# Optimization experiments

Hardware: AMD Instinct MI355X
Metric: run time of the kernel (lower is better)

The kernel has to match this reference:

```python
import jax, jax.numpy as jnp
import numpy as np

H = 256      # hidden_dim
MEL = 80     # num_mel
R = 5        # reduction_factor
BS = 128
T_ENC = 512
T_DEC = 1000


def _gru_step(x, h, wih, whh, bih, bhh):
    # PyTorch GRU cell: gates order (r, z, n)
    gi = x @ wih.T + bih            # [bs, 3H]
    gh = h @ whh.T + bhh
    ir, iz, inn = jnp.split(gi, 3, axis=-1)
    hr, hz, hn = jnp.split(gh, 3, axis=-1)
    r = jax.nn.sigmoid(ir + hr)
    z = jax.nn.sigmoid(iz + hz)
    n = jnp.tanh(inn + r * hn)
    return (1.0 - z) * n + z * h


def setup_inputs() -> dict:
    key = jax.random.key(0)
    ks = iter(jax.random.split(key, 40))
    s = 0.05
    def w(shape):
        return jax.random.normal(next(ks), shape, dtype=jnp.float32) * s
    inp = {
        "enc_vec": jax.random.normal(next(ks), (BS, T_ENC, H), dtype=jnp.float32),
        "decoder_input": jax.random.normal(next(ks), (BS, T_DEC, MEL), dtype=jnp.float32),
        # Pre_net
        "pre_w1": w((H, MEL)), "pre_b1": jnp.zeros((H,), jnp.float32),
        "pre_w2": w((H // 2, H)), "pre_b2": jnp.zeros((H // 2,), jnp.float32),
        # Bahdanau attention
        "w1": w((H, H)), "b1": jnp.zeros((H,), jnp.float32),
        "w2": w((H, H)), "b2": jnp.zeros((H,), jnp.float32),
        "v_w": w((1, H)), "v_b": jnp.zeros((1,), jnp.float32),
        # projection and output
        "proj_w": w((H, 2 * H)), "proj_b": jnp.zeros((H,), jnp.float32),
        "out_w": w((MEL * R, H)), "out_b": jnp.zeros((MEL * R,), jnp.float32),
        # Attention GRU (input H//2)
        "att_wih": w((3 * H, H // 2)), "att_whh": w((3 * H, H)),
        "att_bih": jnp.zeros((3 * H,), jnp.float32), "att_bhh": jnp.zeros((3 * H,), jnp.float32),
        # GRU1, GRU2 (input H)
        "g1_wih": w((3 * H, H)), "g1_whh": w((3 * H, H)),
        "g1_bih": jnp.zeros((3 * H,), jnp.float32), "g1_bhh": jnp.zeros((3 * H,), jnp.float32),
        "g2_wih": w((3 * H, H)), "g2_whh": w((3 * H, H)),
        "g2_bih": jnp.zeros((3 * H,), jnp.float32), "g2_bhh": jnp.zeros((3 * H,), jnp.float32),
    }
    return inp


def reference(enc_vec, decoder_input, pre_w1, pre_b1, pre_w2, pre_b2,
              w1, b1, w2, b2, v_w, v_b, proj_w, proj_b, out_w, out_b,
              att_wih, att_whh, att_bih, att_bhh,
              g1_wih, g1_whh, g1_bih, g1_bhh,
              g2_wih, g2_whh, g2_bih, g2_bhh):
    bs = enc_vec.shape[0]
    # Pre_net (dropout omitted -> deterministic eval behavior)
    pre = jax.nn.relu(decoder_input @ pre_w1.T + pre_b1)
    pre = jax.nn.relu(pre @ pre_w2.T + pre_b2)          # [bs, T_dec, H//2]
    steps = decoder_input.shape[1] // R                 # 200
    # teacher-forced inputs: step i uses pre[:, i*R, :]
    xs = jnp.transpose(pre[:, :steps * R:R, :], (1, 0, 2))   # [steps, bs, H//2]
    # hoist W1(enc_vec): constant across decoder steps
    w1enc = enc_vec @ w1.T + b1                         # [bs, T_enc, H]

    h0 = jnp.zeros((bs, H), jnp.float32)

    def step(carry, x):
        ha, h1, h2 = carry
        d = _gru_step(x, ha, att_wih, att_whh, att_bih, att_bhh)   # [bs, H]
        e = jnp.tanh(w1enc + (d @ w2.T + b2)[:, None, :])          # [bs, T_enc, H]
        scores = e @ v_w[0] + v_b[0]                               # [bs, T_enc]
        u = jax.nn.softmax(scores, axis=1)
        d_dot = jnp.einsum('bt,bth->bh', u, enc_vec)               # [bs, H]
        p = jnp.concatenate([d, d_dot], axis=-1) @ proj_w.T + proj_b  # [bs, H]
        o1 = _gru_step(p, h1, g1_wih, g1_whh, g1_bih, g1_bhh)
        in2 = o1 + p
        o2 = _gru_step(in2, h2, g2_wih, g2_whh, g2_bih, g2_bhh)
        out = (in2 + o2) @ out_w.T + out_b                         # [bs, R*MEL]
        return (d, o1, o2), out

    _, ys = jax.lax.scan(step, (h0, h0, h0), xs)        # [steps, bs, R*MEL]
    ys = jnp.transpose(ys, (1, 0, 2)).reshape(bs, steps * R, MEL)
    return ys
```

## Files before the change

kernel.cpp:

```cpp
#include <hip/hip_runtime.h>
#include <hip/hip_bf16.h>

typedef unsigned short u16;
typedef unsigned int   u32;

constexpr int H     = 256;
constexpr int HH    = 128;
constexpr int MELD  = 80;
constexpr int RF    = 5;
constexpr int BS    = 128;
constexpr int TENC  = 512;
constexpr int TDEC  = 1000;
constexpr int STEPS = 200;
constexpr int OD    = 400;
constexpr int M_ALL = STEPS * BS;

constexpr size_t GI_B   = 0;
constexpr size_t ENC16_B= GI_B;
constexpr size_t D16_B  = GI_B   + (size_t)M_ALL*768*4;
constexpr size_t IN2_B  = D16_B;
constexpr size_t W1ET_B = D16_B  + (size_t)M_ALL*512*2;
constexpr size_t P16_B  = W1ET_B;
constexpr size_t IN2H_B = W1ET_B + (size_t)M_ALL*256*2;
constexpr size_t P_B    = W1ET_B + (size_t)BS*H*TENC*2;
constexpr size_t XSH_B  = P_B    + (size_t)M_ALL*256*4;
constexpr size_t ST16_B = XSH_B  + (size_t)M_ALL*128*2;
constexpr size_t WPK_B  = ST16_B + (size_t)M_ALL*256*2;
constexpr size_t WH_B   = WPK_B  + 3*(size_t)393216;
constexpr size_t WH_AW  = 0;
constexpr size_t WH_W2  = WH_AW + 98304*2;
constexpr size_t WH_PJ  = WH_W2 + 65536*2;
constexpr size_t WH_G1  = WH_PJ + 131072*2;
constexpr size_t WH_G2  = WH_G1 + 196608*2;
constexpr size_t WH_OW  = WH_G2 + 196608*2;
constexpr size_t WH_W1  = WH_OW + 102400*2;
constexpr size_t WH_END = WH_W1 + 65536*2;
constexpr size_t NEED_FAST = WH_B + WH_END;

constexpr size_t FBW1E_B  = 65536;
constexpr size_t FBXST_B  = FBW1E_B + (size_t)BS*TENC*H*2;
constexpr size_t FBF32_B  = FBXST_B + (size_t)STEPS*HH*BS*2;
constexpr size_t FBDT_F   = 0;
constexpr size_t FBO1_F   = FBDT_F + 2*(size_t)H*BS;
constexpr size_t FBO2_F   = FBO1_F + 2*(size_t)H*BS;
constexpr size_t FBPT_F   = FBO2_F + 2*(size_t)H*BS;
constexpr size_t FBIN2_F  = FBPT_F + (size_t)H*BS;
constexpr size_t FBST_F   = FBIN2_F + (size_t)H*BS;
constexpr size_t FB_NEED_B = FBF32_B + (FBST_F + 2*(size_t)H*BS) * 4;

__device__ __forceinline__ float bf2f(u16 v) {
  union { u32 x; float f; } c; c.x = ((u32)v) << 16; return c.f;
}
__device__ __forceinline__ float bfu_lo(u32 u) { union { u32 x; float f; } c; c.x = u << 16;        return c.f; }
__device__ __forceinline__ float bfu_hi(u32 u) { union { u32 x; float f; } c; c.x = u & 0xffff0000u; return c.f; }
__device__ __forceinline__ u16 f2bf(float f) {
  union { float f; u32 u; } c; c.f = f;
  u32 u = c.u;
  u32 r = (u + 0x7fffu + ((u >> 16) & 1u)) >> 16;
  return (u16)r;
}
__device__ __forceinline__ u16 f2h(float f) {
  union { _Float16 h; u16 u; } c; c.h = (_Float16)f; return c.u;
}
__device__ __forceinline__ float fexp(float x) {
  return __builtin_amdgcn_exp2f(1.4426950408889634f * x);
}
__device__ __forceinline__ float sigm_f(float x) {
  return __builtin_amdgcn_rcpf(1.0f + __builtin_amdgcn_exp2f(-1.4426950408889634f * x));
}
__device__ __forceinline__ float tanh_f(float x) {
  x = fminf(fmaxf(x, -15.f), 15.f);
  float e = __builtin_amdgcn_exp2f(2.8853900817779268f * x);
  return (e - 1.0f) * __builtin_amdgcn_rcpf(e + 1.0f);
}

typedef _Float16 hlf2 __attribute__((ext_vector_type(2)));
typedef _Float16 f16x8 __attribute__((ext_vector_type(8)));
typedef float f32x4 __attribute__((ext_vector_type(4)));
#if __has_builtin(__builtin_amdgcn_fdot2)
__device__ __forceinline__ float dot2h(float acc, u32 w, u32 h) {
  union { u32 u; hlf2 v; } cw, ch; cw.u = w; ch.u = h;
  return __builtin_amdgcn_fdot2(cw.v, ch.v, acc, false);
}
#else
__device__ __forceinline__ float dot2h(float acc, u32 w, u32 h) {
  union { u32 u; _Float16 f[2]; } cw, ch; cw.u = w; ch.u = h;
  return acc + (float)cw.f[0] * (float)ch.f[0] + (float)cw.f[1] * (float)ch.f[1];
}
#endif
__device__ __forceinline__ void dot8h(float& acc, const uint4 w, const uint4 hp) {
  acc = dot2h(acc, w.x, hp.x);
  acc = dot2h(acc, w.y, hp.y);
  acc = dot2h(acc, w.z, hp.z);
  acc = dot2h(acc, w.w, hp.w);
}

__global__ __launch_bounds__(256) void k_zero(float* __restrict__ out, int n) {
  int i = blockIdx.x * 256 + threadIdx.x;
  if (i < n) out[i] = 0.f;
}


__global__ __launch_bounds__(256) void k_prenet_f(
    const float* __restrict__ dec, const float* __restrict__ w1, const float* __restrict__ b1,
    const float* __restrict__ w2, const float* __restrict__ b2, u16* __restrict__ xsh)
{
  const int s = blockIdx.x, tid = threadIdx.x;
  __shared__ float X0[32][80];
  __shared__ float P1t[32][256];
  for (int bt = 0; bt < 4; ++bt) {
    const int b0 = bt * 32;
    __syncthreads();
    for (int i = tid; i < 32 * 80; i += 256) {
      int bb = i / 80, m = i - bb * 80;
      X0[bb][m] = dec[((size_t)(b0 + bb) * TDEC + (size_t)s * RF) * MELD + m];
    }
    __syncthreads();
    {
      const int h = tid;
      float acc[32];
      const float bias = b1[h];
      #pragma unroll
      for (int r = 0; r < 32; ++r) acc[r] = bias;
      const float* wr = w1 + (size_t)h * MELD;
      for (int m = 0; m < 80; m += 4) {
        float4 wv = *(const float4*)(wr + m);
        #pragma unroll
        for (int r = 0; r < 32; ++r) {
          float4 x = *(const float4*)&X0[r][m];
          acc[r] += x.x * wv.x + x.y * wv.y + x.z * wv.z + x.w * wv.w;
        }
      }
      #pragma unroll
      for (int r = 0; r < 32; ++r) P1t[r][h] = fmaxf(acc[r], 0.f);
    }
    __syncthreads();
    {
      const int k = tid & 127, bh = tid >> 7;
      float acc[16];
      const float bias = b2[k];
      #pragma unroll
      for (int r = 0; r < 16; ++r) acc[r] = bias;
      const float* wr = w2 + (size_t)k * H;
      for (int h = 0; h < H; h += 4) {
        float4 wv = *(const float4*)(wr + h);
        #pragma unroll
        for (int r = 0; r < 16; ++r) {
          float4 x = *(const float4*)&P1t[bh * 16 + r][h];
          acc[r] += x.x * wv.x + x.y * wv.y + x.z * wv.z + x.w * wv.w;
        }
      }
      #pragma unroll
      for (int r = 0; r < 16; ++r)
        xsh[((size_t)s * BS + b0 + bh * 16 + r) * HH + k] = f2h(fmaxf(acc[r], 0.f));
    }
  }
}

__global__ __launch_bounds__(256) void k_packall(
    const float* __restrict__ enc, u16* __restrict__ enc16,
    const float* __restrict__ awhh, const float* __restrict__ g1whh,
    const float* __restrict__ g2whh, u32* __restrict__ wpk,
    const float* __restrict__ awih, u16* __restrict__ awih16,
    const float* __restrict__ w2w,  u16* __restrict__ w2w16,
    const float* __restrict__ pjw,  u16* __restrict__ pjw16,
    const float* __restrict__ g1wih, u16* __restrict__ g1w16,
    const float* __restrict__ g2wih, u16* __restrict__ g2w16,
    const float* __restrict__ ow,   u16* __restrict__ ow16,
    const float* __restrict__ w1w,  u16* __restrict__ w1w16)
{
  int i = blockIdx.x * 256 + threadIdx.x;
  if (i < 16777216) { enc16[i] = f2h(enc[i]); return; }
  i -= 16777216;
  if (i < 294912) {
    int which = i / 98304, idx = i - which * 98304;
    const float* w = which == 0 ? awhh : (which == 1 ? g1whh : g2whh);
    int ii = idx & 3;
    int j  = (idx >> 2) & 255;
    int k4 = (idx >> 10) & 31;
    int g  = idx >> 15;
    int k2 = 4 * k4 + ii;
    union { _Float16 f[2]; u32 u; } c;
    c.f[0] = (_Float16)w[((size_t)g * 256 + j) * 256 + 2 * k2];
    c.f[1] = (_Float16)w[((size_t)g * 256 + j) * 256 + 2 * k2 + 1];
    wpk[which * 98304 + idx] = c.u;
    return;
  }
  i -= 294912;
  if (i < 98304)  { awih16[i] = f2h(awih[i]); return; }  i -= 98304;
  if (i < 65536)  { w2w16[i]  = f2h(w2w[i]);  return; }  i -= 65536;
  if (i < 131072) { pjw16[i]  = f2h(pjw[i]);  return; }  i -= 131072;
  if (i < 196608) { g1w16[i]  = f2h(g1wih[i]); return; } i -= 196608;
  if (i < 196608) { g2w16[i]  = f2h(g2wih[i]); return; } i -= 196608;
  if (i < 102400) { ow16[i]   = f2h(ow[i]);   return; }  i -= 102400;
  if (i < 65536)  { w1w16[i]  = f2h(w1w[i]);  return; }
}
constexpr int PACKALL_N = 16777216 + 294912 + 856064;

__global__ __launch_bounds__(256) void k_hgemm(
    const u16* __restrict__ A, int lda,
    const u16* __restrict__ W, int K,
    const float* __restrict__ bias,
    float* __restrict__ C, u16* __restrict__ Ch, int ldc, int N,
    float* __restrict__ outmap, u16* __restrict__ CbfT)
{
  __shared__ _Float16 As[128 * 40];
  __shared__ _Float16 Ws[64 * 40];
  const int m0 = blockIdx.y * 128, n0 = blockIdx.x * 64;
  const int tid = threadIdx.x;
  const int wv = tid >> 6, lane = tid & 63;
  const int l15 = lane & 15, hi = lane >> 4;
  f32x4 acc[2][4];
  #pragma unroll
  for (int mi = 0; mi < 2; ++mi)
    #pragma unroll
    for (int ni = 0; ni < 4; ++ni) acc[mi][ni] = (f32x4){0.f, 0.f, 0.f, 0.f};

  const int ar = tid >> 1, ac = (tid & 1) * 16;
  const int wr = tid >> 2, wc = (tid & 3) * 8;
  for (int k0 = 0; k0 < K; k0 += 32) {
    __syncthreads();
    {
      const u16* src = A + (size_t)(m0 + ar) * lda + k0 + ac;
      uint4 v0 = *(const uint4*)(src);
      uint4 v1 = *(const uint4*)(src + 8);
      *(uint4*)&As[ar * 40 + ac] = v0;
      *(uint4*)&As[ar * 40 + ac + 8] = v1;
    }
    {
      uint4 v;
      if (n0 + wr < N) v = *(const uint4*)(W + (size_t)(n0 + wr) * K + k0 + wc);
      else { v.x = v.y = v.z = v.w = 0u; }
      *(uint4*)&Ws[wr * 40 + wc] = v;
    }
    __syncthreads();
    f16x8 af[2], bf[4];
    #pragma unroll
    for (int mi = 0; mi < 2; ++mi)
      af[mi] = *(const f16x8*)&As[(wv * 32 + mi * 16 + l15) * 40 + hi * 8];
    #pragma unroll
    for (int ni = 0; ni < 4; ++ni)
      bf[ni] = *(const f16x8*)&Ws[(ni * 16 + l15) * 40 + hi * 8];
    #pragma unroll
    for (int mi = 0; mi < 2; ++mi)
      #pragma unroll
      for (int ni = 0; ni < 4; ++ni)
        acc[mi][ni] = __builtin_amdgcn_mfma_f32_16x16x32_f16(af[mi], bf[ni], acc[mi][ni], 0, 0, 0);
  }
  const int gm = m0 + wv * 32;
  #pragma unroll
  for (int ni = 0; ni < 4; ++ni) {
    const int col = n0 + ni * 16 + l15;
    if (col < N) {
      const float bv = bias[col];
      #pragma unroll
      for (int mi = 0; mi < 2; ++mi) {
        #pragma unroll
        for (int r = 0; r < 4; ++r) {
          const int row = gm + mi * 16 + hi * 4 + r;
          float v = acc[mi][ni][r] + bv;
          if (outmap) {
            int s = row >> 7, b = row & 127;
            int fr = s * RF + col / MELD, mel = col - (col / MELD) * MELD;
            outmap[((size_t)b * TDEC + fr) * MELD + mel] = v;
          } else if (CbfT) {
            float a = fminf(fmaxf(2.8853900817779268f * v, -15.f), 15.f);
            CbfT[(((size_t)(row >> 9) * 256 + col) << 9) + (row & 511)] =
                f2bf(__builtin_amdgcn_exp2f(a));
          } else {
            if (C)  C[(size_t)row * ldc + col] = v;
            if (Ch) Ch[(size_t)row * ldc + col] = f2h(v);
          }
        }
      }
    }
  }
}

constexpr int KC4H = 2;
constexpr int RG4H = 14;
__global__ __launch_bounds__(512) void k_chain(
    const float* __restrict__ gi,
    const uint4* __restrict__ wpk4,
    const float* __restrict__ bhh,
    const float* __restrict__ addsrc,
    int astride,
    float* __restrict__ outp, int ostride,
    u16* __restrict__ outph, int ostrideh)
{
  const int b = blockIdx.x, tid = threadIdx.x;
  const int j = tid & 255, kh = tid >> 8;
  __shared__ __align__(16) _Float16 hf[256];
  __shared__ float psum[3][256];
  __shared__ uint4 wl4[3][2 * KC4H][256];
  for (int i = tid; i < 3 * 2 * KC4H * 256; i += 512) {
    int g = i / (2 * KC4H * 256), rem = i - g * (2 * KC4H * 256);
    int slot = rem >> 8, jj = rem & 255;
    int c = slot < KC4H ? slot : slot - KC4H;
    int k4 = (slot < KC4H ? 0 : 16) + c;
    wl4[g][slot][jj] = wpk4[((size_t)g * 32 + k4) * 256 + jj];
  }
  uint4 wreg[3][RG4H];
  #pragma unroll
  for (int g = 0; g < 3; ++g) {
    #pragma unroll
    for (int t = 0; t < RG4H; ++t) {
      const int k4 = kh * 16 + KC4H + t;
      wreg[g][t] = wpk4[((size_t)g * 32 + k4) * 256 + j];
    }
  }
  if (tid < 256) hf[tid] = (_Float16)0.f;
  float hreg = 0.f;
  const float br = bhh[j], bz = bhh[256 + j], bn = bhh[512 + j];
  float gr = 0.f, gz = 0.f, gn = 0.f, av = 0.f;
  if (kh == 0) {
    const float* gim = gi + (size_t)b * 768;
    gr = gim[j]; gz = gim[256 + j]; gn = gim[512 + j];
    if (addsrc) av = addsrc[(size_t)b * astride + j];
  }
  __syncthreads();
  for (int s = 0; s < STEPS; ++s) {
    float gr_n = 0.f, gz_n = 0.f, gn_n = 0.f, av_n = 0.f;
    if (kh == 0 && s + 1 < STEPS) {
      const size_t mn = (size_t)(s + 1) * BS + b;
      const float* gim = gi + mn * 768;
      gr_n = gim[j]; gz_n = gim[256 + j]; gn_n = gim[512 + j];
      if (addsrc) av_n = addsrc[mn * astride + j];
    }
    float ar = 0.f, az = 0.f, an = 0.f;
    const int k4b = kh * 16;
    #pragma unroll
    for (int t = 0; t < RG4H; ++t) {
      const int k4 = k4b + KC4H + t;
      uint4 hp = *(const uint4*)&hf[8 * k4];
      dot8h(ar, wreg[0][t], hp); dot8h(az, wreg[1][t], hp); dot8h(an, wreg[2][t], hp);
    }
    #pragma unroll
    for (int c = 0; c < KC4H; ++c) {
      const int k4 = k4b + c;
      const int slot = kh * KC4H + c;
      uint4 hp = *(const uint4*)&hf[8 * k4];
      dot8h(ar, wl4[0][slot][j], hp); dot8h(az, wl4[1][slot][j], hp); dot8h(an, wl4[2][slot][j], hp);
    }
    if (kh == 1) { psum[0][j] = ar; psum[1][j] = az; psum[2][j] = an; }
    __syncthreads();
    if (kh == 0) {
      const size_t m = (size_t)s * BS + b;
      ar += psum[0][j]; az += psum[1][j]; an += psum[2][j];
      float r = sigm_f(gr + ar + br);
      float z = sigm_f(gz + az + bz);
      float n = tanh_f(gn + r * (an + bn));
      float hn_ = (1.f - z) * n + z * hreg;
      hreg = hn_;
      hf[j] = (_Float16)hn_;
      float ov = hn_ + av;
      if (outp)  outp[m * ostride + j] = ov;
      if (outph) outph[m * ostrideh + j] = f2h(ov);
    }
    __syncthreads();
    gr = gr_n; gz = gz_n; gn = gn_n; av = av_n;
  }
}

constexpr int ATT_ST = 10;
__global__ __launch_bounds__(256) void k_att(
    const u16* __restrict__ w1eT, const float* __restrict__ Q,
    const float* __restrict__ vw_, const float* __restrict__ enc,
    u16* __restrict__ D16)
{
  const int b = blockIdx.x, s0 = blockIdx.y * ATT_ST, tid = threadIdx.x;
  __shared__ float qt[ATT_ST][260];
  __shared__ float vws[256];
  __shared__ float us[ATT_ST][516];
  __shared__ float redw[ATT_ST][4];
  vws[tid] = -2.0f * vw_[tid];
  #pragma unroll
  for (int si = 0; si < ATT_ST; ++si) {
    float q = 2.8853900817779268f * Q[((size_t)(s0 + si) * BS + b) * H + tid];
    qt[si][tid] = __builtin_amdgcn_exp2f(fminf(fmaxf(q, -15.f), 15.f));
  }
  __syncthreads();

  float sc0[ATT_ST], sc1[ATT_ST];
  #pragma unroll
  for (int si = 0; si < ATT_ST; ++si) { sc0[si] = 0.f; sc1[si] = 0.f; }
  const u32* wrow = (const u32*)w1eT + (size_t)b * H * (TENC / 2);
  for (int h = 0; h < H; h += 4) {
    u32 wa = wrow[(size_t)(h + 0) * 256 + tid];
    u32 wb = wrow[(size_t)(h + 1) * 256 + tid];
    u32 wc = wrow[(size_t)(h + 2) * 256 + tid];
    u32 wd = wrow[(size_t)(h + 3) * 256 + tid];
    float Ea0 = bfu_lo(wa), Ea1 = bfu_hi(wa);
    float Eb0 = bfu_lo(wb), Eb1 = bfu_hi(wb);
    float Ec0 = bfu_lo(wc), Ec1 = bfu_hi(wc);
    float Ed0 = bfu_lo(wd), Ed1 = bfu_hi(wd);
    float4 vv = *(const float4*)&vws[h];
    #pragma unroll
    for (int si = 0; si < ATT_ST; ++si) {
      float4 Eq = *(const float4*)&qt[si][h];
      {
        float F1 = __builtin_fmaf(Ea0, Eq.x, 1.f);
        float F2 = __builtin_fmaf(Eb0, Eq.y, 1.f);
        float F3 = __builtin_fmaf(Ec0, Eq.z, 1.f);
        float F4 = __builtin_fmaf(Ed0, Eq.w, 1.f);
        float P12 = F1 * F2, P34 = F3 * F4;
        float u12 = __builtin_fmaf(vv.y, F1, vv.x * F2);
        float u34 = __builtin_fmaf(vv.w, F3, vv.z * F4);
        float num = __builtin_fmaf(P12, u34, P34 * u12);
        sc0[si] = __builtin_fmaf(num, __builtin_amdgcn_rcpf(P12 * P34), sc0[si]);
      }
      {
        float F1 = __builtin_fmaf(Ea1, Eq.x, 1.f);
        float F2 = __builtin_fmaf(Eb1, Eq.y, 1.f);
        float F3 = __builtin_fmaf(Ec1, Eq.z, 1.f);
        float F4 = __builtin_fmaf(Ed1, Eq.w, 1.f);
        float P12 = F1 * F2, P34 = F3 * F4;
        float u12 = __builtin_fmaf(vv.y, F1, vv.x * F2);
        float u34 = __builtin_fmaf(vv.w, F3, vv.z * F4);
        float num = __builtin_fmaf(P12, u34, P34 * u12);
        sc1[si] = __builtin_fmaf(num, __builtin_amdgcn_rcpf(P12 * P34), sc1[si]);
      }
    }
  }
  const int lane = tid & 63, wvi = tid >> 6;
  #pragma unroll
  for (int si = 0; si < ATT_ST; ++si) {
    float mw = fmaxf(sc0[si], sc1[si]);
    for (int off = 1; off < 64; off <<= 1) mw = fmaxf(mw, __shfl_xor(mw, off));
    if (lane == 0) redw[si][wvi] = mw;
  }
  __syncthreads();
  #pragma unroll
  for (int si = 0; si < ATT_ST; ++si) {
    float mx = fmaxf(fmaxf(redw[si][0], redw[si][1]), fmaxf(redw[si][2], redw[si][3]));
    sc0[si] = fexp(sc0[si] - mx);
    sc1[si] = fexp(sc1[si] - mx);
  }
  __syncthreads();
  #pragma unroll
  for (int si = 0; si < ATT_ST; ++si) {
    float sm = sc0[si] + sc1[si];
    for (int off = 1; off < 64; off <<= 1) sm += __shfl_xor(sm, off);
    if (lane == 0) redw[si][wvi] = sm;
  }
  __syncthreads();
  #pragma unroll
  for (int si = 0; si < ATT_ST; ++si) {
    float tot = redw[si][0] + redw[si][1] + redw[si][2] + redw[si][3];
    float li = __builtin_amdgcn_rcpf(tot);
    float2 uv; uv.x = sc0[si] * li; uv.y = sc1[si] * li;
    *(float2*)&us[si][2 * tid] = uv;
  }
  __syncthreads();
  float dd[ATT_ST];
  #pragma unroll
  for (int si = 0; si < ATT_ST; ++si) dd[si] = 0.f;
  const float* ep = enc + (size_t)b * TENC * H + tid;
  for (int t = 0; t < TENC; t += 4) {
    float e0 = ep[(size_t)(t + 0) * H];
    float e1 = ep[(size_t)(t + 1) * H];
    float e2 = ep[(size_t)(t + 2) * H];
    float e3 = ep[(size_t)(t + 3) * H];
    #pragma unroll
    for (int si = 0; si < ATT_ST; ++si) {
      float4 u4 = *(const float4*)&us[si][t];
      dd[si] += e0 * u4.x + e1 * u4.y + e2 * u4.z + e3 * u4.w;
    }
  }
  #pragma unroll
  for (int si = 0; si < ATT_ST; ++si)
    D16[((size_t)(s0 + si) * BS + b) * 512 + 256 + tid] = f2h(dd[si]);
}

__global__ __launch_bounds__(256) void fbk_zeroinit(float* __restrict__ fst) {
  int i = blockIdx.x * 256 + threadIdx.x;
  if (i < H * BS)              fst[FBDT_F + i] = 0.f;
  else if (i < 2 * H * BS)     fst[FBO1_F + (i - H * BS)] = 0.f;
  else if (i < 3 * H * BS)     fst[FBO2_F + (i - 2 * H * BS)] = 0.f;
}

__global__ __launch_bounds__(256) void fbk_prenet(
    const float* __restrict__ dec, const float* __restrict__ w1, const float* __restrict__ b1,
    const float* __restrict__ w2, const float* __restrict__ b2, u16* __restrict__ xsT)
{
  const int s = blockIdx.x, tid = threadIdx.x;
  __shared__ float X0[32][80];
  __shared__ float P1t[32][256];
  for (int bt = 0; bt < 4; ++bt) {
    const int b0 = bt * 32;
    __syncthreads();
    for (int i = tid; i < 32 * 80; i += 256) {
      int bb = i / 80, m = i - bb * 80;
      X0[bb][m] = dec[((size_t)(b0 + bb) * TDEC + (size_t)s * RF) * MELD + m];
    }
    __syncthreads();
    {
      const int h = tid;
      float acc[32];
      const float bias = b1[h];
      #pragma unroll
      for (int r = 0; r < 32; ++r) acc[r] = bias;
      const float* wr = w1 + (size_t)h * MELD;
      for (int m = 0; m < 80; m += 4) {
        float4 wv = *(const float4*)(wr + m);
        #pragma unroll
        for (int r = 0; r < 32; ++r) {
          float4 x = *(const float4*)&X0[r][m];
          acc[r] += x.x * wv.x + x.y * wv.y + x.z * wv.z + x.w * wv.w;
        }
      }
      #pragma unroll
      for (int r = 0; r < 32; ++r) P1t[r][h] = fmaxf(acc[r], 0.f);
    }
    __syncthreads();
    {
      const int k = tid & 127, bh = tid >> 7;
      float acc[16];
      const float bias = b2[k];
      #pragma unroll
      for (int r = 0; r < 16; ++r) acc[r] = bias;
      const float* wr = w2 + (size_t)k * H;
      for (int h = 0; h < H; h += 4) {
        float4 wv = *(const float4*)(wr + h);
        #pragma unroll
        for (int r = 0; r < 16; ++r) {
          float4 x = *(const float4*)&P1t[bh * 16 + r][h];
          acc[r] += x.x * wv.x + x.y * wv.y + x.z * wv.z + x.w * wv.w;
        }
      }
      #pragma unroll
      for (int r = 0; r < 16; ++r)
        xsT[((size_t)s * HH + k) * BS + b0 + bh * 16 + r] = f2bf(fmaxf(acc[r], 0.f));
    }
  }
}

__global__ __launch_bounds__(256) void fbk_w1enc(
    const float* __restrict__ enc, const float* __restrict__ w1, const float* __restrict__ b1,
    u16* __restrict__ w1e)
{
  const int row0 = blockIdx.x * 32;
  const int tid = threadIdx.x;
  __shared__ float A[32 * 256];
  for (int i = tid * 4; i < 32 * 256; i += 256 * 4) {
    float4 v = *(const float4*)(enc + (size_t)row0 * H + i);
    A[i] = v.x; A[i + 1] = v.y; A[i + 2] = v.z; A[i + 3] = v.w;
  }
  __syncthreads();
  const int h = tid;
  float acc[32];
  const float bias = b1[h];
  #pragma unroll
  for (int r = 0; r < 32; ++r) acc[r] = bias;
  const float* wr = w1 + (size_t)h * H;
  for (int k = 0; k < H; k += 4) {
    float4 wv = *(const float4*)(wr + k);
    #pragma unroll
    for (int r = 0; r < 32; ++r) {
      float4 a = *(const float4*)&A[r * 256 + k];
      acc[r] += a.x * wv.x + a.y * wv.y + a.z * wv.z + a.w * wv.w;
    }
  }
  #pragma unroll
  for (int r = 0; r < 32; ++r) w1e[((size_t)row0 + r) * H + h] = f2bf(acc[r]);
}

__device__ __forceinline__ void fb_gru_body(
    float (*w6)[260], float (*pA)[128], float (*pB)[128], int j, int tid,
    const float* __restrict__ gi_src, const float* __restrict__ h_src,
    const float* __restrict__ wih, const float* __restrict__ whh,
    const float* __restrict__ bih, const float* __restrict__ bhh,
    float* __restrict__ h_out, float* __restrict__ sum_out)
{
  for (int i = tid; i < 3 * H; i += 256) {
    int gg = i >> 8, k = i & 255;
    w6[gg][k]     = wih[((size_t)gg * H + j) * H + k];
    w6[3 + gg][k] = whh[((size_t)gg * H + j) * H + k];
  }
  __syncthreads();
  const int b = tid & 127, kh = tid >> 7;
  float pr = 0, pz = 0, pn = 0, hr = 0, hz = 0, hn = 0;
  for (int k = kh * 128; k < kh * 128 + 128; k += 4) {
    float4 wia = *(const float4*)&w6[0][k];
    float4 wib = *(const float4*)&w6[1][k];
    float4 wic = *(const float4*)&w6[2][k];
    float4 wha = *(const float4*)&w6[3][k];
    float4 whb = *(const float4*)&w6[4][k];
    float4 whc = *(const float4*)&w6[5][k];
    float x0 = gi_src[(size_t)(k + 0) * BS + b], x1 = gi_src[(size_t)(k + 1) * BS + b];
    float x2 = gi_src[(size_t)(k + 2) * BS + b], x3 = gi_src[(size_t)(k + 3) * BS + b];
    float h0 = h_src[(size_t)(k + 0) * BS + b],  h1 = h_src[(size_t)(k + 1) * BS + b];
    float h2 = h_src[(size_t)(k + 2) * BS + b],  h3 = h_src[(size_t)(k + 3) * BS + b];
    pr += x0 * wia.x + x1 * wia.y + x2 * wia.z + x3 * wia.w;
    pz += x0 * wib.x + x1 * wib.y + x2 * wib.z + x3 * wib.w;
    pn += x0 * wic.x + x1 * wic.y + x2 * wic.z + x3 * wic.w;
    hr += h0 * wha.x + h1 * wha.y + h2 * wha.z + h3 * wha.w;
    hz += h0 * whb.x + h1 * whb.y + h2 * whb.z + h3 * whb.w;
    hn += h0 * whc.x + h1 * whc.y + h2 * whc.z + h3 * whc.w;
  }
  if (kh) {
    pA[0][b] = pr; pA[1][b] = pz; pA[2][b] = pn;
    pB[0][b] = hr; pB[1][b] = hz; pB[2][b] = hn;
  }
  __syncthreads();
  if (!kh) {
    float gir = pr + pA[0][b] + bih[j];
    float giz = pz + pA[1][b] + bih[H + j];
    float gin = pn + pA[2][b] + bih[2 * H + j];
    float ghr = hr + pB[0][b] + bhh[j];
    float ghz = hz + pB[1][b] + bhh[H + j];
    float ghn = hn + pB[2][b] + bhh[2 * H + j];
    float r = sigm_f(gir + ghr);
    float z = sigm_f(giz + ghz);
    float n = tanh_f(gin + r * ghn);
    float hp = h_src[(size_t)j * BS + b];
    float o = (1.f - z) * n + z * hp;
    h_out[(size_t)j * BS + b] = o;
    if (sum_out) sum_out[(size_t)j * BS + b] = o + gi_src[(size_t)j * BS + b];
  }
}

__global__ __launch_bounds__(256) void fbk_attgru(
    const u16* __restrict__ xstu, float* __restrict__ fst,
    const float* __restrict__ awih, const float* __restrict__ awhh,
    const float* __restrict__ abih, const float* __restrict__ abhh, int s)
{
  const int j = blockIdx.x, tid = threadIdx.x;
  __shared__ float w6[6][260];
  __shared__ float pA[3][128];
  __shared__ float pB[3][128];
  const float* dprev = fst + FBDT_F + (size_t)(s & 1) * H * BS;
  float*       dcur  = fst + FBDT_F + (size_t)((s + 1) & 1) * H * BS;
  for (int i = tid; i < 3 * HH; i += 256) {
    int gg = i >> 7, k = i & (HH - 1);
    w6[gg][k] = awih[((size_t)gg * H + j) * HH + k];
  }
  for (int i = tid; i < 3 * H; i += 256) {
    int gg = i >> 8, k = i & (H - 1);
    w6[3 + gg][k] = awhh[((size_t)gg * H + j) * H + k];
  }
  __syncthreads();
  const u16* xcol = xstu + (size_t)s * HH * BS;
  const int b = tid & 127, kh = tid >> 7;
  float pr = 0, pz = 0, pn = 0, hr = 0, hz = 0, hn = 0;
  for (int k = kh * 64; k < kh * 64 + 64; k += 4) {
    float4 wa = *(const float4*)&w6[0][k];
    float4 wb = *(const float4*)&w6[1][k];
    float4 wc = *(const float4*)&w6[2][k];
    float x0 = bf2f(xcol[(size_t)(k + 0) * BS + b]), x1 = bf2f(xcol[(size_t)(k + 1) * BS + b]);
    float x2 = bf2f(xcol[(size_t)(k + 2) * BS + b]), x3 = bf2f(xcol[(size_t)(k + 3) * BS + b]);
    pr += x0 * wa.x + x1 * wa.y + x2 * wa.z + x3 * wa.w;
    pz += x0 * wb.x + x1 * wb.y + x2 * wb.z + x3 * wb.w;
    pn += x0 * wc.x + x1 * wc.y + x2 * wc.z + x3 * wc.w;
  }
  for (int k = kh * 128; k < kh * 128 + 128; k += 4) {
    float4 wa = *(const float4*)&w6[3][k];
    float4 wb = *(const float4*)&w6[4][k];
    float4 wc = *(const float4*)&w6[5][k];
    float h0 = dprev[(size_t)(k + 0) * BS + b], h1 = dprev[(size_t)(k + 1) * BS + b];
    float h2 = dprev[(size_t)(k + 2) * BS + b], h3 = dprev[(size_t)(k + 3) * BS + b];
    hr += h0 * wa.x + h1 * wa.y + h2 * wa.z + h3 * wa.w;
    hz += h0 * wb.x + h1 * wb.y + h2 * wb.z + h3 * wb.w;
    hn += h0 * wc.x + h1 * wc.y + h2 * wc.z + h3 * wc.w;
  }
  if (kh) {
    pA[0][b] = pr; pA[1][b] = pz; pA[2][b] = pn;
    pB[0][b] = hr; pB[1][b] = hz; pB[2][b] = hn;
  }
  __syncthreads();
  if (!kh) {
    float gir = pr + pA[0][b] + abih[j];
    float giz = pz + pA[1][b] + abih[H + j];
    float gin = pn + pA[2][b] + abih[2 * H + j];
    float ghr = hr + pB[0][b] + abhh[j];
    float ghz = hz + pB[1][b] + abhh[H + j];
    float ghn = hn + pB[2][b] + abhh[2 * H + j];
    float r = sigm_f(gir + ghr);
    float z = sigm_f(giz + ghz);
    float n = tanh_f(gin + r * ghn);
    float hp = dprev[(size_t)j * BS + b];
    dcur[(size_t)j * BS + b] = (1.f - z) * n + z * hp;
  }
}

__global__ __launch_bounds__(256) void fbk_attn(
    const float* __restrict__ enc, const u16* __restrict__ w1eu,
    const float* __restrict__ w2w, const float* __restrict__ b2w,
    const float* __restrict__ vww, const float* __restrict__ vbw,
    const float* __restrict__ pjw, const float* __restrict__ pjb,
    float* __restrict__ fst, int s)
{
  const int b3 = blockIdx.x, tid = threadIdx.x;
  __shared__ float dsh[256], qs[256], ddh[256], vwsh[256], ev[512], red[256];
  const float* dcur = fst + FBDT_F + (size_t)((s + 1) & 1) * H * BS;
  float* pT = fst + FBPT_F;
  dsh[tid]  = dcur[(size_t)tid * BS + b3];
  vwsh[tid] = vww[tid];
  __syncthreads();
  {
    const int jj = tid;
    const float* wr = w2w + (size_t)jj * H;
    float acc = b2w[jj];
    for (int k = 0; k < H; k += 8) {
      float4 wA = *(const float4*)(wr + k);
      float4 wB = *(const float4*)(wr + k + 4);
      float4 dA = *(const float4*)&dsh[k];
      float4 dB = *(const float4*)&dsh[k + 4];
      acc += dA.x * wA.x + dA.y * wA.y + dA.z * wA.z + dA.w * wA.w
           + dB.x * wB.x + dB.y * wB.y + dB.z * wB.z + dB.w * wB.w;
    }
    qs[jj] = acc;
  }
  __syncthreads();
  const float vbf = vbw[0];
  const u16* wr0 = w1eu + ((size_t)b3 * TENC + tid) * H;
  const u16* wr1 = wr0 + (size_t)256 * H;
  float sc0 = vbf, sc1 = vbf;
  for (int h = 0; h < H; h += 8) {
    uint4 ua = *(const uint4*)(wr0 + h);
    uint4 uc = *(const uint4*)(wr1 + h);
    float4 qA = *(const float4*)&qs[h];
    float4 qB = *(const float4*)&qs[h + 4];
    float4 vA = *(const float4*)&vwsh[h];
    float4 vB = *(const float4*)&vwsh[h + 4];
    sc0 += vA.x * tanh_f(bfu_lo(ua.x) + qA.x) + vA.y * tanh_f(bfu_hi(ua.x) + qA.y)
         + vA.z * tanh_f(bfu_lo(ua.y) + qA.z) + vA.w * tanh_f(bfu_hi(ua.y) + qA.w)
         + vB.x * tanh_f(bfu_lo(ua.z) + qB.x) + vB.y * tanh_f(bfu_hi(ua.z) + qB.y)
         + vB.z * tanh_f(bfu_lo(ua.w) + qB.z) + vB.w * tanh_f(bfu_hi(ua.w) + qB.w);
    sc1 += vA.x * tanh_f(bfu_lo(uc.x) + qA.x) + vA.y * tanh_f(bfu_hi(uc.x) + qA.y)
         + vA.z * tanh_f(bfu_lo(uc.y) + qA.z) + vA.w * tanh_f(bfu_hi(uc.y) + qA.w)
         + vB.x * tanh_f(bfu_lo(uc.z) + qB.x) + vB.y * tanh_f(bfu_hi(uc.z) + qB.y)
         + vB.z * tanh_f(bfu_lo(uc.w) + qB.z) + vB.w * tanh_f(bfu_hi(uc.w) + qB.w);
  }
  red[tid] = fmaxf(sc0, sc1);
  __syncthreads();
  for (int off = 128; off > 0; off >>= 1) {
    if (tid < off) red[tid] = fmaxf(red[tid], red[tid + off]);
    __syncthreads();
  }
  float mx = red[0];
  __syncthreads();
  float e0 = fexp(sc0 - mx), e1 = fexp(sc1 - mx);
  ev[tid] = e0; ev[256 + tid] = e1;
  red[tid] = e0 + e1;
  __syncthreads();
  for (int off = 128; off > 0; off >>= 1) {
    if (tid < off) red[tid] += red[tid + off];
    __syncthreads();
  }
  float linv = __builtin_amdgcn_rcpf(red[0]);
  __syncthreads();
  {
    float vacc = 0.f;
    const float* ep = enc + (size_t)b3 * TENC * H + tid;
    for (int tt = 0; tt < TENC; tt += 4) {
      float4 e4 = *(const float4*)&ev[tt];
      vacc += e4.x * ep[(size_t)(tt + 0) * H] + e4.y * ep[(size_t)(tt + 1) * H]
            + e4.z * ep[(size_t)(tt + 2) * H] + e4.w * ep[(size_t)(tt + 3) * H];
    }
    ddh[tid] = vacc * linv;
  }
  __syncthreads();
  {
    const int jj = tid;
    const float* wr = pjw + (size_t)jj * (2 * H);
    float acc = pjb[jj];
    for (int k = 0; k < H; k += 8) {
      float4 wA = *(const float4*)(wr + k);
      float4 wB = *(const float4*)(wr + k + 4);
      float4 dA = *(const float4*)&dsh[k];
      float4 dB = *(const float4*)&dsh[k + 4];
      acc += dA.x * wA.x + dA.y * wA.y + dA.z * wA.z + dA.w * wA.w
           + dB.x * wB.x + dB.y * wB.y + dB.z * wB.z + dB.w * wB.w;
    }
    for (int k = 0; k < H; k += 8) {
      float4 wA = *(const float4*)(wr + H + k);
      float4 wB = *(const float4*)(wr + H + k + 4);
      float4 dA = *(const float4*)&ddh[k];
      float4 dB = *(const float4*)&ddh[k + 4];
      acc += dA.x * wA.x + dA.y * wA.y + dA.z * wA.z + dA.w * wA.w
           + dB.x * wB.x + dB.y * wB.y + dB.z * wB.z + dB.w * wB.w;
    }
    pT[(size_t)jj * BS + b3] = acc;
  }
}

__global__ __launch_bounds__(256) void fbk_gru1(
    float* __restrict__ fst,
    const float* __restrict__ wih, const float* __restrict__ whh,
    const float* __restrict__ bih, const float* __restrict__ bhh, int s)
{
  __shared__ float w6[6][260];
  __shared__ float pA[3][128];
  __shared__ float pB[3][128];
  const float* pT     = fst + FBPT_F;
  const float* o1prev = fst + FBO1_F + (size_t)(s & 1) * H * BS;
  float*       o1cur  = fst + FBO1_F + (size_t)((s + 1) & 1) * H * BS;
  float*       in2T   = fst + FBIN2_F;
  fb_gru_body(w6, pA, pB, blockIdx.x, threadIdx.x, pT, o1prev, wih, whh, bih, bhh, o1cur, in2T);
}

__device__ __forceinline__ void fb_out_body(
    float (*pA)[128], int bb, int tid, int s,
    const float* __restrict__ sT, const float* __restrict__ ow,
    const float* __restrict__ ob, float* __restrict__ out)
{
  const int b = tid & 127, kh = tid >> 7;
  for (int r = bb; r < OD; r += 128) {
    const float* wr = ow + (size_t)r * H + kh * 128;
    float acc = 0.f;
    for (int kk = 0; kk < 128; kk += 4) {
      float4 wv = *(const float4*)(wr + kk);
      const float* sp = sT + (size_t)(kh * 128 + kk) * BS + b;
      acc += sp[0] * wv.x + sp[BS] * wv.y + sp[2 * BS] * wv.z + sp[3 * BS] * wv.w;
    }
    __syncthreads();
    if (kh) pA[0][b] = acc;
    __syncthreads();
    if (!kh) {
      float y = acc + pA[0][b] + ob[r];
      int frame = s * RF + r / MELD;
      int m = r - (r / MELD) * MELD;
      out[((size_t)b * TDEC + frame) * MELD + m] = y;
    }
  }
}

__global__ __launch_bounds__(256) void fbk_gru2out(
    float* __restrict__ fst,
    const float* __restrict__ wih, const float* __restrict__ whh,
    const float* __restrict__ bih, const float* __restrict__ bhh,
    const float* __restrict__ ow, const float* __restrict__ ob,
    float* __restrict__ out, int s)
{
  const int bid = blockIdx.x, tid = threadIdx.x;
  __shared__ float w6[6][260];
  __shared__ float pA[3][128];
  __shared__ float pB[3][128];
  if (bid < 256) {
    const float* in2T   = fst + FBIN2_F;
    const float* o2prev = fst + FBO2_F + (size_t)(s & 1) * H * BS;
    float*       o2cur  = fst + FBO2_F + (size_t)((s + 1) & 1) * H * BS;
    float*       stp    = fst + FBST_F + (size_t)(s & 1) * H * BS;
    fb_gru_body(w6, pA, pB, bid, tid, in2T, o2prev, wih, whh, bih, bhh, o2cur, stp);
  } else if (s > 0) {
    const float* sT = fst + FBST_F + (size_t)((s - 1) & 1) * H * BS;
    fb_out_body(pA, bid - 256, tid, s - 1, sT, ow, ob, out);
  }
}

__global__ __launch_bounds__(256) void fbk_outlast(
    const float* __restrict__ fst, const float* __restrict__ ow,
    const float* __restrict__ ob, float* __restrict__ out)
{
  __shared__ float pA[3][128];
  const float* sT = fst + FBST_F + (size_t)((STEPS - 1) & 1) * H * BS;
  fb_out_body(pA, blockIdx.x, threadIdx.x, STEPS - 1, sT, ow, ob, out);
}

extern "C" void kernel_launch(void* const* d_in, const int* in_sizes, int n_in,
                              void* d_out, int out_size, void* d_ws, size_t ws_size,
                              hipStream_t stream) {
  const float* enc   = (const float*)d_in[0];
  const float* dec   = (const float*)d_in[1];
  const float* pw1   = (const float*)d_in[2];
  const float* pb1   = (const float*)d_in[3];
  const float* pw2   = (const float*)d_in[4];
  const float* pb2   = (const float*)d_in[5];
  const float* w1w   = (const float*)d_in[6];
  const float* b1w   = (const float*)d_in[7];
  const float* w2w   = (const float*)d_in[8];
  const float* b2w   = (const float*)d_in[9];
  const float* vww   = (const float*)d_in[10];
  const float* vbw   = (const float*)d_in[11];
  const float* pjw   = (const float*)d_in[12];
  const float* pjb   = (const float*)d_in[13];
  const float* ow    = (const float*)d_in[14];
  const float* ob    = (const float*)d_in[15];
  const float* awih  = (const float*)d_in[16];
  const float* awhh  = (const float*)d_in[17];
  const float* abih  = (const float*)d_in[18];
  const float* abhh  = (const float*)d_in[19];
  const float* g1wih = (const float*)d_in[20];
  const float* g1whh = (const float*)d_in[21];
  const float* g1bih = (const float*)d_in[22];
  const float* g1bhh = (const float*)d_in[23];
  const float* g2wih = (const float*)d_in[24];
  const float* g2whh = (const float*)d_in[25];
  const float* g2bih = (const float*)d_in[26];
  const float* g2bhh = (const float*)d_in[27];
  float* out = (float*)d_out;
  char* wsb = (char*)d_ws;

  if (ws_size >= NEED_FAST) {
    float* GI   = (float*)(wsb + GI_B);
    u16*   ENC16= (u16*)(wsb + ENC16_B);
    u16*   D16  = (u16*)(wsb + D16_B);
    float* IN2  = (float*)(wsb + IN2_B);
    u16*   w1eT = (u16*)(wsb + W1ET_B);
    u16*   P16  = (u16*)(wsb + P16_B);
    u16*   IN2H = (u16*)(wsb + IN2H_B);
    float* P    = (float*)(wsb + P_B);
    u16*   XSH  = (u16*)(wsb + XSH_B);
    u16*   ST16 = (u16*)(wsb + ST16_B);
    u32*   wpkA = (u32*)(wsb + WPK_B);
    u32*   wpk1 = wpkA + 98304;
    u32*   wpk2 = wpk1 + 98304;
    u16*   awih16 = (u16*)(wsb + WH_B + WH_AW);
    u16*   w2w16  = (u16*)(wsb + WH_B + WH_W2);
    u16*   pjw16  = (u16*)(wsb + WH_B + WH_PJ);
    u16*   g1w16  = (u16*)(wsb + WH_B + WH_G1);
    u16*   g2w16  = (u16*)(wsb + WH_B + WH_G2);
    u16*   ow16   = (u16*)(wsb + WH_B + WH_OW);
    u16*   w1w16  = (u16*)(wsb + WH_B + WH_W1);

    k_packall<<<PACKALL_N / 256, 256, 0, stream>>>(
        enc, ENC16, awhh, g1whh, g2whh, wpkA,
        awih, awih16, w2w, w2w16, pjw, pjw16, g1wih, g1w16,
        g2wih, g2w16, ow, ow16, w1w, w1w16);
    k_hgemm<<<dim3(4, (BS * TENC) / 128), 256, 0, stream>>>(
        ENC16, H, w1w16, H, b1w, nullptr, nullptr, 0, 256, nullptr, w1eT);
    k_prenet_f<<<STEPS, 256, 0, stream>>>(dec, pw1, pb1, pw2, pb2, XSH);
    k_hgemm<<<dim3(12, M_ALL / 128), 256, 0, stream>>>(XSH, HH, awih16, HH, abih, GI, nullptr, 768, 768, nullptr, nullptr);
    k_chain<<<BS, 512, 0, stream>>>(GI, (const uint4*)wpkA, abhh, nullptr, 0, nullptr, 0, D16, 512);
    k_hgemm<<<dim3(4, M_ALL / 128), 256, 0, stream>>>(D16, 512, w2w16, H, b2w, GI, nullptr, 256, 256, nullptr, nullptr);
    k_att<<<dim3(BS, STEPS / ATT_ST), 256, 0, stream>>>(w1eT, GI, vww, enc, D16);
    k_hgemm<<<dim3(4, M_ALL / 128), 256, 0, stream>>>(D16, 512, pjw16, 2 * H, pjb, P, P16, 256, 256, nullptr, nullptr);
    k_hgemm<<<dim3(12, M_ALL / 128), 256, 0, stream>>>(P16, H, g1w16, H, g1bih, GI, nullptr, 768, 768, nullptr, nullptr);
    k_chain<<<BS, 512, 0, stream>>>(GI, (const uint4*)wpk1, g1bhh, P, 256, IN2, 256, IN2H, 256);
    k_hgemm<<<dim3(12, M_ALL / 128), 256, 0, stream>>>(IN2H, H, g2w16, H, g2bih, GI, nullptr, 768, 768, nullptr, nullptr);
    k_chain<<<BS, 512, 0, stream>>>(GI, (const uint4*)wpk2, g2bhh, IN2, 256, nullptr, 0, ST16, 256);
    k_hgemm<<<dim3(7, M_ALL / 128), 256, 0, stream>>>(ST16, H, ow16, H, ob, nullptr, nullptr, 0, OD, out, nullptr);
    return;
  }

  if (ws_size < FB_NEED_B) {
    k_zero<<<(out_size + 255) / 256, 256, 0, stream>>>(out, out_size);
    return;
  }

  u16*  w1eu = (u16*)(wsb + FBW1E_B);
  u16*  xstu = (u16*)(wsb + FBXST_B);
  float* fst = (float*)(wsb + FBF32_B);

  fbk_zeroinit<<<384, 256, 0, stream>>>(fst);
  fbk_prenet<<<STEPS, 256, 0, stream>>>(dec, pw1, pb1, pw2, pb2, xstu);
  fbk_w1enc<<<(BS * TENC) / 32, 256, 0, stream>>>(enc, w1w, b1w, w1eu);
  for (int s = 0; s < STEPS; ++s) {
    fbk_attgru<<<256, 256, 0, stream>>>(xstu, fst, awih, awhh, abih, abhh, s);
    fbk_attn<<<BS, 256, 0, stream>>>(enc, w1eu, w2w, b2w, vww, vbw, pjw, pjb, fst, s);
    fbk_gru1<<<256, 256, 0, stream>>>(fst, g1wih, g1whh, g1bih, g1bhh, s);
    fbk_gru2out<<<384, 256, 0, stream>>>(fst, g2wih, g2whh, g2bih, g2bhh, ow, ob, out, s);
  }
  fbk_outlast<<<BS, 256, 0, stream>>>(fst, ow, ob, out);
}
```

Before: 1.754 ms.

## Move attention context reduction out of k_att into batched MFMA GEMM

Result: faster. 1.615 ms (-8.0%).

```diff
diff --git a/kernel.cpp b/kernel.cpp
--- a/kernel.cpp
+++ b/kernel.cpp
@@ -23,6 +23,7 @@
 constexpr size_t P16_B  = W1ET_B;
 constexpr size_t IN2H_B = W1ET_B + (size_t)M_ALL*256*2;
 constexpr size_t P_B    = W1ET_B + (size_t)BS*H*TENC*2;
+constexpr size_t U16_B  = P_B;
 constexpr size_t XSH_B  = P_B    + (size_t)M_ALL*256*4;
 constexpr size_t ST16_B = XSH_B  + (size_t)M_ALL*128*2;
 constexpr size_t WPK_B  = ST16_B + (size_t)M_ALL*256*2;
@@ -277,6 +278,77 @@
   }
 }
 
+__global__ __launch_bounds__(256) void k_ddgemm(
+    const u16* __restrict__ U, const float* __restrict__ enc,
+    u16* __restrict__ D16)
+{
+  __shared__ _Float16 As[128 * 40];
+  __shared__ _Float16 Ws[64 * 40];
+  const int b = blockIdx.z;
+  const int m0 = blockIdx.y * 128, n0 = blockIdx.x * 64;
+  const int tid = threadIdx.x;
+  const int wv = tid >> 6, lane = tid & 63;
+  const int l15 = lane & 15, hi = lane >> 4;
+  f32x4 acc[2][4];
+  #pragma unroll
+  for (int mi = 0; mi < 2; ++mi)
+    #pragma unroll
+    for (int ni = 0; ni < 4; ++ni) acc[mi][ni] = (f32x4){0.f, 0.f, 0.f, 0.f};
+
+  const u16* A = U + (size_t)b * STEPS * TENC;
+  const float* E = enc + (size_t)b * TENC * H;
+  const int ar = tid >> 1, ac = (tid & 1) * 16;
+  for (int k0 = 0; k0 < TENC; k0 += 32) {
+    __syncthreads();
+    {
+      const u16* src = A + (size_t)(m0 + ar) * TENC + k0 + ac;
+      uint4 v0 = *(const uint4*)(src);
+      uint4 v1 = *(const uint4*)(src + 8);
+      *(uint4*)&As[ar * 40 + ac] = v0;
+      *(uint4*)&As[ar * 40 + ac + 8] = v1;
+    }
+    {
+      #pragma unroll
+      for (int it = 0; it < 2; ++it) {
+        int flat = tid + it * 256;
+        int kk = flat >> 4, hc4 = (flat & 15) * 4;
+        float4 v = *(const float4*)(E + (size_t)(k0 + kk) * H + n0 + hc4);
+        Ws[(hc4 + 0) * 40 + kk] = (_Float16)v.x;
+        Ws[(hc4 + 1) * 40 + kk] = (_Float16)v.y;
+        Ws[(hc4 + 2) * 40 + kk] = (_Float16)v.z;
+        Ws[(hc4 + 3) * 40 + kk] = (_Float16)v.w;
+      }
+    }
+    __syncthreads();
+    f16x8 af[2], bf[4];
+    #pragma unroll
+    for (int mi = 0; mi < 2; ++mi)
+      af[mi] = *(const f16x8*)&As[(wv * 32 + mi * 16 + l15) * 40 + hi * 8];
+    #pragma unroll
+    for (int ni = 0; ni < 4; ++ni)
+      bf[ni] = *(const f16x8*)&Ws[(ni * 16 + l15) * 40 + hi * 8];
+    #pragma unroll
+    for (int mi = 0; mi < 2; ++mi)
+      #pragma unroll
+      for (int ni = 0; ni < 4; ++ni)
+        acc[mi][ni] = __builtin_amdgcn_mfma_f32_16x16x32_f16(af[mi], bf[ni], acc[mi][ni], 0, 0, 0);
+  }
+  const int gm = m0 + wv * 32;
+  #pragma unroll
+  for (int ni = 0; ni < 4; ++ni) {
+    const int col = n0 + ni * 16 + l15;
+    #pragma unroll
+    for (int mi = 0; mi < 2; ++mi) {
+      #pragma unroll
+      for (int r = 0; r < 4; ++r) {
+        const int row = gm + mi * 16 + hi * 4 + r;
+        if (row < STEPS)
+          D16[((size_t)(row * BS + b)) * 512 + 256 + col] = f2h(acc[mi][ni][r]);
+      }
+    }
+  }
+}
+
 constexpr int KC4H = 2;
 constexpr int RG4H = 14;
 __global__ __launch_bounds__(512) void k_chain(
@@ -365,13 +437,11 @@
 constexpr int ATT_ST = 10;
 __global__ __launch_bounds__(256) void k_att(
     const u16* __restrict__ w1eT, const float* __restrict__ Q,
-    const float* __restrict__ vw_, const float* __restrict__ enc,
-    u16* __restrict__ D16)
+    const float* __restrict__ vw_, u16* __restrict__ U16)
 {
   const int b = blockIdx.x, s0 = blockIdx.y * ATT_ST, tid = threadIdx.x;
   __shared__ float qt[ATT_ST][260];
   __shared__ float vws[256];
-  __shared__ float us[ATT_ST][516];
   __shared__ float redw[ATT_ST][4];
   vws[tid] = -2.0f * vw_[tid];
   #pragma unroll
@@ -448,28 +518,9 @@
   for (int si = 0; si < ATT_ST; ++si) {
     float tot = redw[si][0] + redw[si][1] + redw[si][2] + redw[si][3];
     float li = __builtin_amdgcn_rcpf(tot);
-    float2 uv; uv.x = sc0[si] * li; uv.y = sc1[si] * li;
-    *(float2*)&us[si][2 * tid] = uv;
-  }
-  __syncthreads();
-  float dd[ATT_ST];
-  #pragma unroll
-  for (int si = 0; si < ATT_ST; ++si) dd[si] = 0.f;
-  const float* ep = enc + (size_t)b * TENC * H + tid;
-  for (int t = 0; t < TENC; t += 4) {
-    float e0 = ep[(size_t)(t + 0) * H];
-    float e1 = ep[(size_t)(t + 1) * H];
-    float e2 = ep[(size_t)(t + 2) * H];
-    float e3 = ep[(size_t)(t + 3) * H];
-    #pragma unroll
-    for (int si = 0; si < ATT_ST; ++si) {
-      float4 u4 = *(const float4*)&us[si][t];
-      dd[si] += e0 * u4.x + e1 * u4.y + e2 * u4.z + e3 * u4.w;
-    }
-  }
-  #pragma unroll
-  for (int si = 0; si < ATT_ST; ++si)
-    D16[((size_t)(s0 + si) * BS + b) * 512 + 256 + tid] = f2h(dd[si]);
+    u32 pk = (u32)f2h(sc0[si] * li) | ((u32)f2h(sc1[si] * li) << 16);
+    *(u32*)&U16[((size_t)b * STEPS + s0 + si) * TENC + 2 * tid] = pk;
+  }
 }
 
 __global__ __launch_bounds__(256) void fbk_zeroinit(float* __restrict__ fst) {
@@ -901,6 +952,7 @@
     u16*   P16  = (u16*)(wsb + P16_B);
     u16*   IN2H = (u16*)(wsb + IN2H_B);
     float* P    = (float*)(wsb + P_B);
+    u16*   U16  = (u16*)(wsb + U16_B);
     u16*   XSH  = (u16*)(wsb + XSH_B);
     u16*   ST16 = (u16*)(wsb + ST16_B);
     u32*   wpkA = (u32*)(wsb + WPK_B);
@@ -924,7 +976,8 @@
     k_hgemm<<<dim3(12, M_ALL / 128), 256, 0, stream>>>(XSH, HH, awih16, HH, abih, GI, nullptr, 768, 768, nullptr, nullptr);
     k_chain<<<BS, 512, 0, stream>>>(GI, (const uint4*)wpkA, abhh, nullptr, 0, nullptr, 0, D16, 512);
     k_hgemm<<<dim3(4, M_ALL / 128), 256, 0, stream>>>(D16, 512, w2w16, H, b2w, GI, nullptr, 256, 256, nullptr, nullptr);
-    k_att<<<dim3(BS, STEPS / ATT_ST), 256, 0, stream>>>(w1eT, GI, vww, enc, D16);
+    k_att<<<dim3(BS, STEPS / ATT_ST), 256, 0, stream>>>(w1eT, GI, vww, U16);
+    k_ddgemm<<<dim3(4, 2, BS), 256, 0, stream>>>(U16, enc, D16);
     k_hgemm<<<dim3(4, M_ALL / 128), 256, 0, stream>>>(D16, 512, pjw16, 2 * H, pjb, P, P16, 256, 256, nullptr, nullptr);
     k_hgemm<<<dim3(12, M_ALL / 128), 256, 0, stream>>>(P16, H, g1w16, H, g1bih, GI, nullptr, 768, 768, nullptr, nullptr);
     k_chain<<<BS, 512, 0, stream>>>(GI, (const uint4*)wpk1, g1bhh, P, 256, IN2, 256, IN2H, 256);
```
